# Kernel tuning notes

Measured on AMD Instinct MI355X. Metric: run time of the kernel, lower is better.

The kernel has to match this reference:

```python
import jax, jax.numpy as jnp
import numpy as np

B, S, D = 8, 2048, 128

def setup_inputs() -> dict:
    key = jax.random.key(0)
    kq, kk, kv, km = jax.random.split(key, 4)
    q = jax.random.normal(kq, (B, S, D), dtype=jnp.float32)
    k = jax.random.normal(kk, (B, S, D), dtype=jnp.float32)
    v = jax.random.normal(kv, (B, S, D), dtype=jnp.float32)
    mask = jax.random.randint(km, (B, S), 0, 2).astype(bool)  # True = masked out
    return {"q": q, "k": k, "v": v, "mask": mask}

def reference(q, k, v, mask):
    scaler = np.sqrt(D).astype(np.float32)
    # score[b, i, j] = <q_i, k_j> / sqrt(d_k)
    score = jnp.einsum('bik,bjk->bij', q, k) / scaler
    score = score - jnp.max(score, axis=-1, keepdims=True)
    e = jnp.exp(score)
    # mask is (B, S_kv): broadcast across query positions, zero out masked keys
    e = jnp.where(mask[:, None, :], 0.0, e)
    a = e / jnp.sum(e, axis=-1, keepdims=True)
    c = jnp.einsum('bij,bjd->bid', a, v)
    return c
```

## Files before the change

### kernel.cpp

```cpp
#include <hip/hip_runtime.h>
#include <hip/hip_fp16.h>
#include <math.h>

typedef __attribute__((ext_vector_type(8))) short short8;
typedef __attribute__((ext_vector_type(16))) float floatx16;
typedef __attribute__((ext_vector_type(2))) __bf16 bf16x2;
typedef __attribute__((ext_vector_type(2))) unsigned int uint2v;

namespace {
constexpr int Bn = 8;
constexpr int Sn = 2048;
constexpr int Dn = 128;
constexpr int BQ = 128;
constexpr int BK = 64;
constexpr int QTILES = Sn / BQ;
constexpr int NKB = Sn / BK;
constexpr int ROWS = Bn * Sn;
constexpr int NSPLIT = 4;
constexpr float SC2 = 0.12753102063642597f;
constexpr float DEFER_THR = 8.0f;
constexpr int TILE_USH = BK * Dn;
}

#if __has_builtin(__builtin_amdgcn_exp2f)
#define EXP2(x) __builtin_amdgcn_exp2f(x)
#else
#define EXP2(x) exp2f(x)
#endif

__device__ __forceinline__ unsigned short f2bf(float x) {
  union { float f; unsigned u; } a; a.f = x;
  unsigned r = a.u + 0x7fffu + ((a.u >> 16) & 1u);
  return (unsigned short)(r >> 16);
}

__device__ __forceinline__ unsigned pack2bf(float x, float y) {
  union { bf16x2 b; unsigned u; } c;
  c.b[0] = (__bf16)x; c.b[1] = (__bf16)y;
  return c.u;
}

__device__ __forceinline__ uint2v pl32swap(unsigned a, unsigned b, int h) {
#if __has_builtin(__builtin_amdgcn_permlane32_swap)
  (void)h;
  return __builtin_amdgcn_permlane32_swap(a, b, false, false);
#else
  unsigned ax = __shfl_xor((int)a, 32);
  unsigned bx = __shfl_xor((int)b, 32);
  uint2v r;
  r[0] = h ? bx : a;
  r[1] = h ? b : ax;
  return r;
#endif
}

__global__ __launch_bounds__(256)
void mask_scan(const unsigned char* __restrict__ mraw,
               unsigned short* __restrict__ idxg, int* __restrict__ cntg) {
  __shared__ int sc[256];
  const int b = blockIdx.x;
  const int t = threadIdx.x;

  unsigned wv = ((const unsigned int*)mraw)[t];
  int any1  = __syncthreads_or((wv & 0x0000ff00u) ? 1 : 0);
  int any23 = __syncthreads_or((wv & 0xffff0000u) ? 1 : 0);
  const int mlayout = any1 ? 1 : (any23 ? 2 : 0);

  const int s0 = t * 8;
  const int gbase = b * Sn + s0;
  bool ms[8];
  if (mlayout == 1) {
    #pragma unroll
    for (int i = 0; i < 8; ++i) ms[i] = mraw[gbase + i] != 0;
  } else if (mlayout == 2) {
    const float* mf = (const float*)mraw;
    #pragma unroll
    for (int i = 0; i < 8; ++i) ms[i] = mf[gbase + i] != 0.0f;
  } else {
    const int* mi = (const int*)mraw;
    #pragma unroll
    for (int i = 0; i < 8; ++i) ms[i] = mi[gbase + i] != 0;
  }

  int c = 0;
  #pragma unroll
  for (int i = 0; i < 8; ++i) c += ms[i] ? 0 : 1;
  sc[t] = c;
  __syncthreads();
  for (int off = 1; off < 256; off <<= 1) {
    int v = (t >= off) ? sc[t - off] : 0;
    __syncthreads();
    sc[t] += v;
    __syncthreads();
  }
  const int incl = sc[t];
  const int total = sc[255];
  int pos = incl - c;
  #pragma unroll
  for (int i = 0; i < 8; ++i)
    if (!ms[i]) idxg[b * Sn + (pos++)] = (unsigned short)(s0 + i);
  if (t == 0) cntg[b] = total;
}

__global__ __launch_bounds__(256)
void prep(const float* __restrict__ kg, const float* __restrict__ vg,
          const unsigned short* __restrict__ idxg, const int* __restrict__ cntg,
          unsigned short* __restrict__ Kpg, unsigned short* __restrict__ Vpg) {
  __shared__ __align__(16) float Vf[16 * 136];
  const int p = blockIdx.x;
  const int b = p >> 7, qq = p & 127;
  const int kb = qq >> 2, k16 = qq & 3;
  const int t = threadIdx.x;

  const int cnt = cntg[b];
  const int padded = (cnt + 63) & ~63;
  const int slot0 = kb * 64 + k16 * 16;
  if (slot0 >= padded) return;

  const int j  = t >> 4;
  const int o8 = t & 15;
  const int sl = slot0 + j;
  const bool real = sl < cnt;

  float4 a, bq, va, vb;
  if (real) {
    const int srow = idxg[b * Sn + sl];
    const size_t base = ((size_t)(b * Sn + srow)) * 32 + o8 * 2;
    a  = ((const float4*)kg)[base]; bq = ((const float4*)kg)[base + 1];
    va = ((const float4*)vg)[base]; vb = ((const float4*)vg)[base + 1];
  } else {
    a = bq = va = vb = make_float4(0.f, 0.f, 0.f, 0.f);
  }

  {
    union { unsigned u[4]; short8 s8; } pk;
    pk.u[0] = pack2bf(a.x, a.y);   pk.u[1] = pack2bf(a.z, a.w);
    pk.u[2] = pack2bf(bq.x, bq.y); pk.u[3] = pack2bf(bq.z, bq.w);
    const int jl = k16 * 16 + j;
    *(short8*)(Kpg + (size_t)(b * NKB + kb) * TILE_USH + jl * 128 + ((o8 ^ (jl & 7)) * 8)) = pk.s8;
  }
  {
    *(float4*)&Vf[j * 136 + o8 * 8]     = va;
    *(float4*)&Vf[j * 136 + o8 * 8 + 4] = vb;
  }
  __syncthreads();
  {
    const int d = t >> 1, h = t & 1;
    union { unsigned u[4]; short8 s8; } pv;
    #pragma unroll
    for (int i = 0; i < 4; ++i)
      pv.u[i] = pack2bf(Vf[(h * 8 + 2 * i) * 136 + d], Vf[(h * 8 + 2 * i + 1) * 136 + d]);
    const int og = k16 * 2 + h;
    *(short8*)(Vpg + (size_t)(b * NKB + kb) * TILE_USH + d * 64 + ((og ^ (d & 7)) * 8)) = pv.s8;
  }
}

template<int SPLIT, bool DIRECT>
__global__ __launch_bounds__(256, 2)
void attn_fwd(const float* __restrict__ qg,
              const unsigned short* __restrict__ Kpg,
              const unsigned short* __restrict__ Vpg,
              const int* __restrict__ cntg,
              float* __restrict__ outg, __half* __restrict__ Op,
              float* __restrict__ Mp, float* __restrict__ Lp) {
  const int tid = threadIdx.x;
  const int bid = blockIdx.x;
  const int b   = bid & 7;
  const int q0  = ((bid >> 3) & (QTILES - 1)) * BQ;
  const int s   = bid >> 7;
  const int w   = tid >> 6;
  const int L   = tid & 63;
  const int q   = L & 31;
  const int h   = L >> 5;
  const int sw  = q & 7;

  const int cnt = cntg[b];
  const int nt  = (cnt + 63) >> 6;
  const int kb0 = (s * nt) / SPLIT;
  const int kbN = ((s + 1) * nt) / SPLIT;
  const int T   = kbN - kb0;

  const int row = b * Sn + q0 + w * 32 + q;

  if (T <= 0) {
    if constexpr (DIRECT) {
      float* orow = outg + (size_t)row * Dn;
      float4 z = make_float4(0.f, 0.f, 0.f, 0.f);
      #pragma unroll
      for (int dg = 0; dg < 4; ++dg)
        #pragma unroll
        for (int ro = 0; ro < 4; ++ro) *(float4*)&orow[dg * 32 + 8 * ro + 4 * h] = z;
    } else {
      __half* orow = Op + ((size_t)s * ROWS + row) * Dn;
      uint2 z; z.x = 0u; z.y = 0u;
      #pragma unroll
      for (int dg = 0; dg < 4; ++dg)
        #pragma unroll
        for (int ro = 0; ro < 4; ++ro) *(uint2*)&orow[dg * 32 + 8 * ro + 4 * h] = z;
      if (h == 0) { Mp[s * ROWS + row] = -INFINITY; Lp[s * ROWS + row] = 0.0f; }
    }
    return;
  }

  const unsigned short* ktile = Kpg + (size_t)b * NKB * TILE_USH;
  const unsigned short* vtile = Vpg + (size_t)b * NKB * TILE_USH;

  short8 qh[8], ql[8];
  {
    const float* qrow = qg + (size_t)row * Dn;
    #pragma unroll
    for (int kstep = 0; kstep < 8; ++kstep) {
      float4 f0 = *(const float4*)(qrow + kstep * 16 + h * 8);
      float4 f1 = *(const float4*)(qrow + kstep * 16 + h * 8 + 4);
      float xs[8] = {f0.x, f0.y, f0.z, f0.w, f1.x, f1.y, f1.z, f1.w};
      #pragma unroll
      for (int j = 0; j < 8; ++j) {
        unsigned short hi = f2bf(xs[j]);
        union { unsigned u; float f; } hv; hv.u = ((unsigned)hi) << 16;
        qh[kstep][j] = (short)hi;
        ql[kstep][j] = (short)f2bf(xs[j] - hv.f);
      }
    }
  }

  float m_i = -INFINITY, l_i = 0.0f;
  float mtrue = -INFINITY;
  floatx16 O32[4];
  #pragma unroll
  for (int dg = 0; dg < 4; ++dg)
    #pragma unroll
    for (int r = 0; r < 16; ++r) O32[dg][r] = 0.0f;

  for (int kb = kb0; kb < kbN; ++kb) {
    const unsigned short* Kc = ktile + (size_t)kb * TILE_USH;
    const unsigned short* Vc = vtile + (size_t)kb * TILE_USH;

    floatx16 sS[2];
    #pragma unroll
    for (int kg = 0; kg < 2; ++kg)
      #pragma unroll
      for (int r = 0; r < 16; ++r) sS[kg][r] = 0.0f;
    #pragma unroll
    for (int kstep = 0; kstep < 8; ++kstep) {
      const int ko = ((kstep * 2 + h) ^ sw) * 8;
      #pragma unroll
      for (int kg = 0; kg < 2; ++kg) {
        short8 kf = *(const short8*)&Kc[(kg * 32 + q) * 128 + ko];
        sS[kg] = __builtin_amdgcn_mfma_f32_32x32x16_bf16(kf, qh[kstep], sS[kg], 0, 0, 0);
        sS[kg] = __builtin_amdgcn_mfma_f32_32x32x16_bf16(kf, ql[kstep], sS[kg], 0, 0, 0);
      }
    }

    if ((kb + 1) * BK <= cnt) {
      #pragma unroll
      for (int kg = 0; kg < 2; ++kg)
        #pragma unroll
        for (int r = 0; r < 16; ++r) sS[kg][r] *= SC2;
    } else {
      #pragma unroll
      for (int kg = 0; kg < 2; ++kg)
        #pragma unroll
        for (int r = 0; r < 16; ++r) {
          const int key = kb * BK + kg * 32 + ((r & 3) + 8 * (r >> 2)) + 4 * h;
          sS[kg] = sS[kg];
          sS[kg][r] = fmaf(sS[kg][r], SC2, (key < cnt) ? 0.0f : -1e30f);
        }
    }
    float mxp[4] = {-INFINITY, -INFINITY, -INFINITY, -INFINITY};
    #pragma unroll
    for (int kg = 0; kg < 2; ++kg)
      #pragma unroll
      for (int r = 0; r < 16; ++r) mxp[r & 3] = fmaxf(mxp[r & 3], sS[kg][r]);
    float mx = fmaxf(fmaxf(mxp[0], mxp[1]), fmaxf(mxp[2], mxp[3]));
    mx = fmaxf(mx, __shfl_xor(mx, 32));
    mtrue = fmaxf(mtrue, mx);

    float mnew;
    if (__all(mx <= m_i + DEFER_THR)) {
      mnew = m_i;
    } else {
      mnew = fmaxf(m_i, mx);
      const float alpha = EXP2(m_i - mnew);
      l_i *= alpha;
      #pragma unroll
      for (int dg = 0; dg < 4; ++dg)
        #pragma unroll
        for (int r = 0; r < 16; ++r) O32[dg][r] *= alpha;
    }

    float rsp[4] = {0.f, 0.f, 0.f, 0.f};
    #pragma unroll
    for (int kg = 0; kg < 2; ++kg)
      #pragma unroll
      for (int r = 0; r < 16; ++r) {
        float e = EXP2(sS[kg][r] - mnew);
        sS[kg][r] = e;
        rsp[r & 3] += e;
      }
    float rs = (rsp[0] + rsp[1]) + (rsp[2] + rsp[3]);
    rs += __shfl_xor(rs, 32);
    l_i += rs;
    m_i = mnew;

    unsigned xw[2][4][2];
    #pragma unroll
    for (int kg = 0; kg < 2; ++kg)
      #pragma unroll
      for (int m = 0; m < 4; ++m) {
        xw[kg][m][0] = pack2bf(sS[kg][4 * m + 0], sS[kg][4 * m + 1]);
        xw[kg][m][1] = pack2bf(sS[kg][4 * m + 2], sS[kg][4 * m + 3]);
      }
    unsigned pfw[4][4];
    #pragma unroll
    for (int kg = 0; kg < 2; ++kg)
      #pragma unroll
      for (int j = 0; j < 2; ++j)
        #pragma unroll
        for (int c2 = 0; c2 < 2; ++c2) {
          uint2v r = pl32swap(xw[kg][2 * j][c2], xw[kg][2 * j + 1][c2], h);
          pfw[kg * 2 + j][c2]     = r[0];
          pfw[kg * 2 + j][2 + c2] = r[1];
        }

    #pragma unroll
    for (int k2 = 0; k2 < 4; ++k2) {
      const int ko = ((k2 * 2 + h) ^ sw) * 8;
      union { unsigned u[4]; short8 s8; } pw;
      pw.u[0] = pfw[k2][0]; pw.u[1] = pfw[k2][1];
      pw.u[2] = pfw[k2][2]; pw.u[3] = pfw[k2][3];
      #pragma unroll
      for (int dg = 0; dg < 4; ++dg) {
        short8 vf = *(const short8*)&Vc[(dg * 32 + q) * 64 + ko];
        O32[dg] = __builtin_amdgcn_mfma_f32_32x32x16_bf16(vf, pw.s8, O32[dg], 0, 0, 0);
      }
    }
  }

  if constexpr (DIRECT) {
    const float inv = 1.0f / l_i;
    float* orow = outg + (size_t)row * Dn;
    #pragma unroll
    for (int dg = 0; dg < 4; ++dg)
      #pragma unroll
      for (int ro = 0; ro < 4; ++ro) {
        float4 f = make_float4(O32[dg][4 * ro] * inv,     O32[dg][4 * ro + 1] * inv,
                               O32[dg][4 * ro + 2] * inv, O32[dg][4 * ro + 3] * inv);
        *(float4*)&orow[dg * 32 + 8 * ro + 4 * h] = f;
      }
  } else {
    const float fin = EXP2(m_i - mtrue);
    __half* orow = Op + ((size_t)s * ROWS + row) * Dn;
    #pragma unroll
    for (int dg = 0; dg < 4; ++dg)
      #pragma unroll
      for (int ro = 0; ro < 4; ++ro) {
        union { __half2 h2[2]; uint2 u; } pk;
        pk.h2[0] = __floats2half2_rn(O32[dg][4 * ro] * fin,     O32[dg][4 * ro + 1] * fin);
        pk.h2[1] = __floats2half2_rn(O32[dg][4 * ro + 2] * fin, O32[dg][4 * ro + 3] * fin);
        *(uint2*)&orow[dg * 32 + 8 * ro + 4 * h] = pk.u;
      }
    if (h == 0) {
      Mp[s * ROWS + row] = mtrue;
      Lp[s * ROWS + row] = l_i * fin;
    }
  }
}

__global__ __launch_bounds__(256)
void attn_combine(const __half* __restrict__ Op, const float* __restrict__ Mp,
                  const float* __restrict__ Lp, float4* __restrict__ out4) {
  const int gid = blockIdx.x * 256 + threadIdx.x;
  const int row = gid >> 5;
  const int c4  = gid & 31;
  float ms[NSPLIT];
  float m = -INFINITY;
  #pragma unroll
  for (int s = 0; s < NSPLIT; ++s) { ms[s] = Mp[s * ROWS + row]; m = fmaxf(m, ms[s]); }
  float l = 0.0f;
  float4 acc = make_float4(0.f, 0.f, 0.f, 0.f);
  #pragma unroll
  for (int s = 0; s < NSPLIT; ++s) {
    float wgt = EXP2(ms[s] - m);
    l = fmaf(Lp[s * ROWS + row], wgt, l);
    union { uint2 u; __half2 h2[2]; } pk;
    pk.u = ((const uint2*)Op)[(size_t)(s * ROWS + row) * 32 + c4];
    float2 f0 = __half22float2(pk.h2[0]);
    float2 f1 = __half22float2(pk.h2[1]);
    acc.x = fmaf(f0.x, wgt, acc.x);
    acc.y = fmaf(f0.y, wgt, acc.y);
    acc.z = fmaf(f1.x, wgt, acc.z);
    acc.w = fmaf(f1.y, wgt, acc.w);
  }
  float inv = 1.0f / l;
  out4[(size_t)row * 32 + c4] = make_float4(acc.x * inv, acc.y * inv, acc.z * inv, acc.w * inv);
}

extern "C" void kernel_launch(void* const* d_in, const int* in_sizes, int n_in,
                              void* d_out, int out_size, void* d_ws, size_t ws_size,
                              hipStream_t stream) {
  const float* q = (const float*)d_in[0];
  const float* k = (const float*)d_in[1];
  const float* v = (const float*)d_in[2];
  const unsigned char* m = (const unsigned char*)d_in[3];
  float* out = (float*)d_out;
  (void)in_sizes; (void)n_in; (void)out_size;

  constexpr size_t OPB = (size_t)NSPLIT * ROWS * Dn * sizeof(__half);
  constexpr size_t MLB = (size_t)NSPLIT * ROWS * sizeof(float);
  constexpr size_t KPB = (size_t)Bn * NKB * TILE_USH * 2;
  constexpr size_t CNTB = 64;
  constexpr size_t IDXB = (size_t)Bn * Sn * sizeof(unsigned short);

  char* ws = (char*)d_ws;
  if (ws_size >= OPB + 2 * MLB + 2 * KPB + CNTB + IDXB) {
    __half* Op = (__half*)ws;
    float* Mp = (float*)(ws + OPB);
    float* Lp = (float*)(ws + OPB + MLB);
    unsigned short* Kp = (unsigned short*)(ws + OPB + 2 * MLB);
    unsigned short* Vp = (unsigned short*)(ws + OPB + 2 * MLB + KPB);
    int* cnt = (int*)(ws + OPB + 2 * MLB + 2 * KPB);
    unsigned short* idx = (unsigned short*)(ws + OPB + 2 * MLB + 2 * KPB + CNTB);
    mask_scan<<<dim3(Bn), dim3(256), 0, stream>>>(m, idx, cnt);
    prep<<<dim3(Bn * NKB * 4), dim3(256), 0, stream>>>(k, v, idx, cnt, Kp, Vp);
    attn_fwd<NSPLIT, false><<<dim3(Bn * QTILES * NSPLIT), dim3(256), 0, stream>>>(
        q, Kp, Vp, cnt, out, Op, Mp, Lp);
    attn_combine<<<dim3(ROWS * 32 / 256), dim3(256), 0, stream>>>(
        Op, Mp, Lp, (float4*)out);
  } else if (ws_size >= 2 * KPB + CNTB + IDXB) {
    unsigned short* Kp = (unsigned short*)ws;
    unsigned short* Vp = (unsigned short*)(ws + KPB);
    int* cnt = (int*)(ws + 2 * KPB);
    unsigned short* idx = (unsigned short*)(ws + 2 * KPB + CNTB);
    mask_scan<<<dim3(Bn), dim3(256), 0, stream>>>(m, idx, cnt);
    prep<<<dim3(Bn * NKB * 4), dim3(256), 0, stream>>>(k, v, idx, cnt, Kp, Vp);
    attn_fwd<1, true><<<dim3(Bn * QTILES), dim3(256), 0, stream>>>(
        q, Kp, Vp, cnt, out, nullptr, nullptr, nullptr);
  }
}
```

Before: 110.2 us.

## Stage K/V tiles into LDS with async global_load_lds multi-buffering

Instead of every wave reading the pre-packed bf16 K and V fragments straight from global memory inside the MFMA loops, the block now copies each tile into shared memory using direct global-to-LDS loads. K uses three buffers and V uses two, with prefetches issued one or two tiles ahead. Waits on the vector-memory counter and block barriers keep the buffers consistent. The goal is to hide global latency and cut redundant per-wave global reads, at the cost of 80KB of LDS per block, which may limit occupancy at two blocks per CU, plus two barriers per iteration.

```diff
diff --git a/kernel.cpp b/kernel.cpp
--- a/kernel.cpp
+++ b/kernel.cpp
@@ -54,6 +54,16 @@
 #endif
 }
 
+__device__ __forceinline__ void gl_lds16(const void* g, void* l, int lane) {
+#if __has_builtin(__builtin_amdgcn_global_load_lds)
+  (void)lane;
+  __builtin_amdgcn_global_load_lds((const __attribute__((address_space(1))) unsigned int*)g,
+                                   (__attribute__((address_space(3))) unsigned int*)l, 16, 0, 0);
+#else
+  *(float4*)((char*)l + lane * 16) = *(const float4*)g;
+#endif
+}
+
 __global__ __launch_bounds__(256)
 void mask_scan(const unsigned char* __restrict__ mraw,
                unsigned short* __restrict__ idxg, int* __restrict__ cntg) {
@@ -155,6 +165,15 @@
   }
 }
 
+__device__ __forceinline__ void stage_tile(const char* gsrc, char* ldst,
+                                           int stagebase, int L) {
+  #pragma unroll
+  for (int i = 0; i < 4; ++i) {
+    const int off = stagebase + i * 1024;
+    gl_lds16(gsrc + off + L * 16, ldst + off, L);
+  }
+}
+
 template<int SPLIT, bool DIRECT>
 __global__ __launch_bounds__(256, 2)
 void attn_fwd(const float* __restrict__ qg,
@@ -163,6 +182,9 @@
               const int* __restrict__ cntg,
               float* __restrict__ outg, __half* __restrict__ Op,
               float* __restrict__ Mp, float* __restrict__ Lp) {
+  __shared__ __align__(16) unsigned short Khi[3][TILE_USH];
+  __shared__ __align__(16) unsigned short Vt[2][TILE_USH];
+
   const int tid = threadIdx.x;
   const int bid = blockIdx.x;
   const int b   = bid & 7;
@@ -202,8 +224,9 @@
     return;
   }
 
-  const unsigned short* ktile = Kpg + (size_t)b * NKB * TILE_USH;
-  const unsigned short* vtile = Vpg + (size_t)b * NKB * TILE_USH;
+  const char* ktile = (const char*)(Kpg + (size_t)b * NKB * TILE_USH);
+  const char* vtile = (const char*)(Vpg + (size_t)b * NKB * TILE_USH);
+  const int stagebase = w * 4096;
 
   short8 qh[8], ql[8];
   {
@@ -231,9 +254,31 @@
     #pragma unroll
     for (int r = 0; r < 16; ++r) O32[dg][r] = 0.0f;
 
+  stage_tile(vtile + (size_t)kb0 * (TILE_USH * 2), (char*)Vt[0], stagebase, L);
+  stage_tile(ktile + (size_t)kb0 * (TILE_USH * 2), (char*)Khi[0], stagebase, L);
+  if (kb0 + 1 < kbN)
+    stage_tile(ktile + (size_t)(kb0 + 1) * (TILE_USH * 2), (char*)Khi[1], stagebase, L);
+
+  int ci3 = 0;
   for (int kb = kb0; kb < kbN; ++kb) {
-    const unsigned short* Kc = ktile + (size_t)kb * TILE_USH;
-    const unsigned short* Vc = vtile + (size_t)kb * TILE_USH;
+    const int i = kb - kb0;
+
+    if (kb + 1 < kbN)
+      stage_tile(vtile + (size_t)(kb + 1) * (TILE_USH * 2),
+                 (char*)Vt[(i + 1) & 1], stagebase, L);
+    int nk3 = ci3 + 2; if (nk3 >= 3) nk3 -= 3;
+    if (kb + 2 < kbN)
+      stage_tile(ktile + (size_t)(kb + 2) * (TILE_USH * 2),
+                 (char*)Khi[nk3], stagebase, L);
+
+    if (kb + 2 < kbN)      asm volatile("s_waitcnt vmcnt(12)" ::: "memory");
+    else if (kb + 1 < kbN) asm volatile("s_waitcnt vmcnt(8)"  ::: "memory");
+    else                   asm volatile("s_waitcnt vmcnt(0)"  ::: "memory");
+    __builtin_amdgcn_s_barrier();
+    asm volatile("" ::: "memory");
+
+    const unsigned short* Kc = Khi[ci3];
+    const unsigned short* Vc = Vt[i & 1];
 
     floatx16 sS[2];
     #pragma unroll
@@ -262,7 +307,6 @@
         #pragma unroll
         for (int r = 0; r < 16; ++r) {
           const int key = kb * BK + kg * 32 + ((r & 3) + 8 * (r >> 2)) + 4 * h;
-          sS[kg] = sS[kg];
           sS[kg][r] = fmaf(sS[kg][r], SC2, (key < cnt) ? 0.0f : -1e30f);
         }
     }
@@ -334,6 +378,10 @@
         O32[dg] = __builtin_amdgcn_mfma_f32_32x32x16_bf16(vf, pw.s8, O32[dg], 0, 0, 0);
       }
     }
+
+    asm volatile("" ::: "memory");
+    __builtin_amdgcn_s_barrier();
+    ci3 = (ci3 == 2) ? 0 : ci3 + 1;
   }
 
   if constexpr (DIRECT) {
```

Result: no change. 108.3 us (-1.7%).
